# Kernel tuning notes

Hardware: AMD Instinct MI355X
Metric: run time of the kernel (lower is better)

The kernel has to match this reference:

```python
import jax, jax.numpy as jnp
import numpy as np

E = 200_000        # num edges (messages)
T = 2_000_000      # num triplets
H = 128            # hidden_channels
I = 64             # int_emb_size
B = 8              # basis_emb_size
NR = 6             # num_radial
NS = 7             # num_spherical
NB_BEFORE = 1
NB_AFTER = 2


def _glorot(key, shape, scale=2.0):
    fan = shape[0] + shape[1]
    std = jnp.sqrt(scale * 2.0 / fan)
    return jax.random.normal(key, shape, dtype=jnp.float32) * std


def setup_inputs() -> dict:
    key = jax.random.key(0)
    ks = jax.random.split(key, 20)
    inp = {
        "x": jax.random.normal(ks[0], (E, H), dtype=jnp.float32),
        "rbf": jax.random.uniform(ks[1], (E, NR), dtype=jnp.float32),
        "sbf": jax.random.uniform(ks[2], (T, NS * NR), dtype=jnp.float32),
        "idx_kj": jax.random.randint(ks[3], (T,), 0, E),
        "idx_ji": jax.random.randint(ks[4], (T,), 0, E),
        # weights stored as [in, out] so forward is x @ W
        "W_rbf1": _glorot(ks[5], (NR, B)),
        "W_rbf2": _glorot(ks[6], (B, H)),
        "W_sbf1": _glorot(ks[7], (NS * NR, B)),
        "W_sbf2": _glorot(ks[8], (B, I)),
        "W_kj": _glorot(ks[9], (H, H)),
        "b_kj": jnp.zeros((H,), dtype=jnp.float32),
        "W_ji": _glorot(ks[10], (H, H)),
        "b_ji": jnp.zeros((H,), dtype=jnp.float32),
        "W_down": _glorot(ks[11], (H, I)),
        "W_up": _glorot(ks[12], (I, H)),
        # residual layers: [n_layers, 2, H, H] weights, [n_layers, 2, H] biases
        "W_res_before": jnp.stack([jnp.stack([_glorot(jax.random.fold_in(ks[13], 2 * l + m), (H, H)) for m in range(2)]) for l in range(NB_BEFORE)]),
        "b_res_before": jnp.zeros((NB_BEFORE, 2, H), dtype=jnp.float32),
        "W_lin": _glorot(ks[14], (H, H)),
        "b_lin": jnp.zeros((H,), dtype=jnp.float32),
        "W_res_after": jnp.stack([jnp.stack([_glorot(jax.random.fold_in(ks[15], 2 * l + m), (H, H)) for m in range(2)]) for l in range(NB_AFTER)]),
        "b_res_after": jnp.zeros((NB_AFTER, 2, H), dtype=jnp.float32),
    }
    return inp


def _residual_stack(h, Ws, bs):
    # h: [E,H]; Ws: [L,2,H,H]; bs: [L,2,H]
    for l in range(Ws.shape[0]):
        inner = jax.nn.silu(h @ Ws[l, 0] + bs[l, 0])
        h = h + jax.nn.silu(inner @ Ws[l, 1] + bs[l, 1])
    return h


def reference(x, rbf, sbf, idx_kj, idx_ji,
              W_rbf1, W_rbf2, W_sbf1, W_sbf2,
              W_kj, b_kj, W_ji, b_ji, W_down, W_up,
              W_res_before, b_res_before, W_lin, b_lin,
              W_res_after, b_res_after):
    act = jax.nn.silu  # swish
    x_ji = act(x @ W_ji + b_ji)                    # [E,H]
    x_kj = act(x @ W_kj + b_kj)                    # [E,H]
    rbf_e = (rbf @ W_rbf1) @ W_rbf2                # [E,H]
    x_kj = x_kj * rbf_e
    x_kj = act(x_kj @ W_down)                      # [E,I]
    sbf_e = (sbf @ W_sbf1) @ W_sbf2                # [T,I]
    m = x_kj[idx_kj] * sbf_e                       # [T,I] gather + basis weight
    agg = jax.ops.segment_sum(m, idx_ji, num_segments=x.shape[0])  # [E,I] scatter-add
    x_kj = act(agg @ W_up)                         # [E,H]
    h = x_ji + x_kj
    h = _residual_stack(h, W_res_before, b_res_before)
    h = act(h @ W_lin + b_lin) + x                 # skip connection
    h = _residual_stack(h, W_res_after, b_res_after)
    return h
```

## Files before the change

kernel.cpp:

```cpp
#include <hip/hip_runtime.h>
#include <math.h>
#include <stdint.h>

#define SCHUNK 2048
#define PCH 128

typedef __bf16 bf16x8 __attribute__((ext_vector_type(8)));
typedef __bf16 bf16x4 __attribute__((ext_vector_type(4)));
typedef float f32x4 __attribute__((ext_vector_type(4)));

#define MFMA16(a, b, c) __builtin_amdgcn_mfma_f32_16x16x32_bf16(a, b, c, 0, 0, 0)

#define OFF_KJ    0
#define OFF_JI    16384
#define OFF_DOWN  32768
#define OFF_UP    40960
#define OFF_RB0   49152
#define OFF_RB1   65536
#define OFF_LIN   81920
#define OFF_RA00  98304
#define OFF_RA01  114688
#define OFF_RA10  131072
#define OFF_RA11  147456

__device__ __forceinline__ float silu_f(float v) {
    return v * __builtin_amdgcn_rcpf(1.0f + __expf(-v));
}

template<int K, int NB, int NT, int STRIDE, int NTOT>
__device__ __forceinline__ void wgemm(const __bf16* __restrict__ At,
                                      const __bf16* __restrict__ Wf,
                                      int ct0, int lane, f32x4* __restrict__ acc) {
#pragma unroll
    for (int i = 0; i < NB * NT; ++i) acc[i] = (f32x4){0.f, 0.f, 0.f, 0.f};
    const int rl = lane & 15;
    const int kq = (lane >> 4) * 8;
    const int sw = (rl & 7) << 3;
#pragma unroll
    for (int kc = 0; kc < K / 32; ++kc) {
        const int k0 = kc * 32 + kq;
        bf16x8 ef[NB];
#pragma unroll
        for (int s = 0; s < NB; ++s)
            ef[s] = *(const bf16x8*)&At[(rl + 16 * s) * STRIDE + (k0 ^ sw)];
#pragma unroll
        for (int t = 0; t < NT; ++t) {
            bf16x8 wf = *(const bf16x8*)&Wf[(size_t)((kc * NTOT + ct0 + t) * 64 + lane) * 8];
#pragma unroll
            for (int s = 0; s < NB; ++s)
                acc[t * NB + s] = MFMA16(wf, ef[s], acc[t * NB + s]);
        }
    }
}

template<int COLS, int NTHR>
__device__ __forceinline__ void stage(const float* __restrict__ g, long grow0,
                                      int vr, __bf16* __restrict__ At, int tid) {
    constexpr int QUADS = COLS / 4;
#pragma unroll
    for (int i = tid; i < 64 * QUADS; i += NTHR) {
        int r = i / QUADS, q = i - r * QUADS;
        float4 v = make_float4(0.f, 0.f, 0.f, 0.f);
        if (r < vr) v = *(const float4*)&g[(grow0 + r) * (size_t)COLS + q * 4];
        bf16x4 w; w[0] = (__bf16)v.x; w[1] = (__bf16)v.y; w[2] = (__bf16)v.z; w[3] = (__bf16)v.w;
        *(bf16x4*)&At[r * 128 + ((q * 4) ^ ((r & 7) << 3))] = w;
    }
}

template<int COLS, int NTHR>
__device__ __forceinline__ void stage_bf(const __bf16* __restrict__ g, long grow0,
                                         int vr, __bf16* __restrict__ At, int tid) {
    constexpr int CH = COLS / 8;
#pragma unroll
    for (int i = tid; i < 64 * CH; i += NTHR) {
        int r = i / CH, q = i - r * CH;
        bf16x8 v = (bf16x8){0, 0, 0, 0, 0, 0, 0, 0};
        if (r < vr) v = *(const bf16x8*)&g[(grow0 + r) * (size_t)COLS + q * 8];
        *(bf16x8*)&At[r * 128 + ((q * 8) ^ ((r & 7) << 3))] = v;
    }
}

__device__ __forceinline__ void epi_store(__bf16* __restrict__ At, const f32x4* __restrict__ acc,
                                          const float* __restrict__ bias, int lane,
                                          int rowbase, int colbase) {
    const int rl = lane & 15, rg = (lane >> 4) << 2;
#pragma unroll
    for (int t = 0; t < 2; ++t) {
        const int cb = colbase + t * 16 + rg;
        const float4 bv = *(const float4*)&bias[cb];
        const float bb[4] = {bv.x, bv.y, bv.z, bv.w};
#pragma unroll
        for (int s = 0; s < 2; ++s) {
            const int el = rowbase + s * 16 + rl;
            bf16x4 w;
#pragma unroll
            for (int j = 0; j < 4; ++j) w[j] = (__bf16)silu_f(acc[t * 2 + s][j] + bb[j]);
            *(bf16x4*)&At[el * 128 + (cb ^ ((el & 7) << 3))] = w;
        }
    }
}

template<bool WRITE>
__device__ __forceinline__ void epi_add(__bf16* __restrict__ At, f32x4* __restrict__ hreg,
                                        const f32x4* __restrict__ acc,
                                        const float* __restrict__ bias, int lane,
                                        int rowbase, int colbase) {
    const int rl = lane & 15, rg = (lane >> 4) << 2;
#pragma unroll
    for (int t = 0; t < 2; ++t) {
        const int cb = colbase + t * 16 + rg;
        const float4 bv = *(const float4*)&bias[cb];
        const float bb[4] = {bv.x, bv.y, bv.z, bv.w};
#pragma unroll
        for (int s = 0; s < 2; ++s) {
            const int el = rowbase + s * 16 + rl;
            bf16x4 w;
#pragma unroll
            for (int j = 0; j < 4; ++j) {
                float v = hreg[t * 2 + s][j] + silu_f(acc[t * 2 + s][j] + bb[j]);
                hreg[t * 2 + s][j] = v;
                w[j] = (__bf16)v;
            }
            if (WRITE) *(bf16x4*)&At[el * 128 + (cb ^ ((el & 7) << 3))] = w;
        }
    }
}

__global__ void kweights(const float* __restrict__ W_rbf1, const float* __restrict__ W_rbf2,
                         const float* __restrict__ W_sbf1, const float* __restrict__ W_sbf2,
                         float* __restrict__ wcrT, float* __restrict__ wc_sbf,
                         __bf16* __restrict__ wcsb) {
    int tid = blockIdx.x * blockDim.x + threadIdx.x;
    int nt = blockDim.x * gridDim.x;
    for (int idx = tid; idx < 128 * 8; idx += nt) {
        int c = idx >> 3, s = idx & 7;
        float v = 0.f;
        if (s < 6) {
#pragma unroll
            for (int b = 0; b < 8; ++b) v += W_rbf1[s * 8 + b] * W_rbf2[b * 128 + c];
        }
        wcrT[idx] = v;
    }
    for (int idx = tid; idx < 42 * 64; idx += nt) {
        int r = idx / 64, c = idx - r * 64;
        float s = 0.f;
#pragma unroll
        for (int b = 0; b < 8; ++b) s += W_sbf1[r * 8 + b] * W_sbf2[b * 64 + c];
        wc_sbf[idx] = s;
    }
    for (int idx = tid; idx < 4096; idx += nt) {
        int j = idx & 7, l = (idx >> 3) & 63, r2 = idx >> 9;
        int ct = r2 & 3, kc = r2 >> 2;
        int k = kc * 32 + ((l >> 4) << 3) + j;
        int c = ct * 16 + (l & 15);
        float v = 0.f;
        if (k < 42) {
#pragma unroll
            for (int b = 0; b < 8; ++b) v += W_sbf1[k * 8 + b] * W_sbf2[b * 64 + c];
        }
        wcsb[idx] = (__bf16)v;
    }
}

__global__ void ktrans(const float* __restrict__ W_kj, const float* __restrict__ W_ji,
                       const float* __restrict__ W_down, const float* __restrict__ W_up,
                       const float* __restrict__ W_rb, const float* __restrict__ W_lin,
                       const float* __restrict__ W_ra, __bf16* __restrict__ wt) {
    const float* src; __bf16* dst; int K, N;
    switch (blockIdx.y) {
        case 0:  src = W_kj;          dst = wt + OFF_KJ;    K = 128; N = 128; break;
        case 1:  src = W_ji;          dst = wt + OFF_JI;    K = 128; N = 128; break;
        case 2:  src = W_down;        dst = wt + OFF_DOWN;  K = 128; N = 64;  break;
        case 3:  src = W_up;          dst = wt + OFF_UP;    K = 64;  N = 128; break;
        case 4:  src = W_rb;          dst = wt + OFF_RB0;   K = 128; N = 128; break;
        case 5:  src = W_rb + 16384;  dst = wt + OFF_RB1;   K = 128; N = 128; break;
        case 6:  src = W_lin;         dst = wt + OFF_LIN;   K = 128; N = 128; break;
        case 7:  src = W_ra;          dst = wt + OFF_RA00;  K = 128; N = 128; break;
        case 8:  src = W_ra + 16384;  dst = wt + OFF_RA01;  K = 128; N = 128; break;
        case 9:  src = W_ra + 32768;  dst = wt + OFF_RA10;  K = 128; N = 128; break;
        default: src = W_ra + 49152;  dst = wt + OFF_RA11;  K = 128; N = 128; break;
    }
    const int ntot = N / 16;
    for (int i = blockIdx.x * blockDim.x + threadIdx.x; i < K * N; i += gridDim.x * blockDim.x) {
        int j = i & 7, l = (i >> 3) & 63, r2 = i >> 9;
        int ct = r2 % ntot, kc = r2 / ntot;
        int k = kc * 32 + ((l >> 4) << 3) + j;
        int n = ct * 16 + (l & 15);
        dst[i] = (__bf16)src[(size_t)k * N + n];
    }
}

__global__ __launch_bounds__(512, 4) void kpre_m(
        const float* __restrict__ x, const float* __restrict__ rbf,
        const __bf16* __restrict__ wt, const float* __restrict__ b_kj,
        const float* __restrict__ wcrT, __bf16* __restrict__ xkd, int E) {
    __shared__ __bf16 A0[64 * 128];
    __shared__ __bf16 A1[64 * 128];
    __shared__ float rbt[64 * 8];
    const int tid = threadIdx.x, lane = tid & 63, wv = tid >> 6;
    const int rh = wv & 1, cq = wv >> 1;
    const int rowbase = rh * 32, colbase = cq * 32;
    const long r0 = (long)blockIdx.x * 64;
    if (r0 >= E) return;
    const int vr = (E - r0) < 64 ? (int)(E - r0) : 64;
    const int rl = lane & 15, rg = (lane >> 4) << 2;

    stage<128, 512>(x, r0, vr, A0, tid);
    for (int i = tid; i < 64 * 8; i += 512) {
        int r = i >> 3, s = i & 7;
        rbt[i] = (s < 6 && r < vr) ? rbf[(r0 + r) * 6 + s] : 0.f;
    }
    __syncthreads();

    f32x4 acc[4];
    wgemm<128, 2, 2, 128, 8>(A0 + rowbase * 128, wt + OFF_KJ, cq * 2, lane, acc);

#pragma unroll
    for (int t = 0; t < 2; ++t) {
        const int cb = colbase + t * 16 + rg;
        const float4 bv = *(const float4*)&b_kj[cb];
        const float bb[4] = {bv.x, bv.y, bv.z, bv.w};
        float wcr[4][6];
#pragma unroll
        for (int j = 0; j < 4; ++j) {
            float4 a4 = *(const float4*)&wcrT[(cb + j) * 8];
            float2 a2 = *(const float2*)&wcrT[(cb + j) * 8 + 4];
            wcr[j][0] = a4.x; wcr[j][1] = a4.y; wcr[j][2] = a4.z;
            wcr[j][3] = a4.w; wcr[j][4] = a2.x; wcr[j][5] = a2.y;
        }
#pragma unroll
        for (int s = 0; s < 2; ++s) {
            const int el = rowbase + s * 16 + rl;
            float4 r4 = *(const float4*)&rbt[el * 8];
            float2 r2 = *(const float2*)&rbt[el * 8 + 4];
            bf16x4 w;
#pragma unroll
            for (int j = 0; j < 4; ++j) {
                float re = r4.x * wcr[j][0] + r4.y * wcr[j][1] + r4.z * wcr[j][2]
                         + r4.w * wcr[j][3] + r2.x * wcr[j][4] + r2.y * wcr[j][5];
                w[j] = (__bf16)(silu_f(acc[t * 2 + s][j] + bb[j]) * re);
            }
            *(bf16x4*)&A1[el * 128 + (cb ^ ((el & 7) << 3))] = w;
        }
    }
    __syncthreads();

    const int hw = wv >> 2, ct = wv & 3;
    const int cb2 = ct * 16 + rg;
    f32x4 acc2[2];
    wgemm<128, 2, 1, 128, 4>(A1 + hw * 32 * 128, wt + OFF_DOWN, ct, lane, acc2);
#pragma unroll
    for (int s = 0; s < 2; ++s) {
        const int el = hw * 32 + s * 16 + rl;
        if (el < vr) {
            bf16x4 w;
#pragma unroll
            for (int j = 0; j < 4; ++j) w[j] = (__bf16)silu_f(acc2[s][j]);
            *(bf16x4*)&xkd[(r0 + el) * 64 + cb2] = w;
        }
    }
}

__global__ __launch_bounds__(512, 4) void kpost_m(
        const float* __restrict__ x, const __bf16* __restrict__ agg,
        const __bf16* __restrict__ mperm, const int* __restrict__ rs,
        const __bf16* __restrict__ wt, const float* __restrict__ b_ji,
        const float* __restrict__ b_rb, const float* __restrict__ b_lin,
        const float* __restrict__ b_ra, float* __restrict__ out, int E,
        int use_mperm) {
    __shared__ __bf16 A0[64 * 128];
    __shared__ __bf16 A1[64 * 128];
    const int tid = threadIdx.x, lane = tid & 63, wv = tid >> 6;
    const int rh = wv & 1, cq = wv >> 1;
    const int rowbase = rh * 32, colbase = cq * 32;
    const int ct0 = cq * 2;
    const long r0 = (long)blockIdx.x * 64;
    if (r0 >= E) return;
    const int vr = (E - r0) < 64 ? (int)(E - r0) : 64;
    const int rl = lane & 15, rg = (lane >> 4) << 2;
    f32x4 acc[4], hreg[4];

    stage<128, 512>(x, r0, vr, A1, tid);

    if (use_mperm) {
        const int el = tid >> 3, oct = tid & 7;
        const long e = r0 + el;
        float s0[8], s1[8];
#pragma unroll
        for (int k = 0; k < 8; ++k) { s0[k] = 0.f; s1[k] = 0.f; }
        if (el < vr) {
            const int j0 = rs[e], j1 = rs[e + 1];
            const __bf16* pm = mperm + (size_t)j0 * 64 + oct * 8;
            const int n = j1 - j0;
            int j = 0;
            for (; j + 2 <= n; j += 2) {
                bf16x8 v0 = *(const bf16x8*)&pm[(size_t)j * 64];
                bf16x8 v1 = *(const bf16x8*)&pm[(size_t)(j + 1) * 64];
#pragma unroll
                for (int k = 0; k < 8; ++k) { s0[k] += (float)v0[k]; s1[k] += (float)v1[k]; }
            }
            if (j < n) {
                bf16x8 v0 = *(const bf16x8*)&pm[(size_t)j * 64];
#pragma unroll
                for (int k = 0; k < 8; ++k) s0[k] += (float)v0[k];
            }
        }
        bf16x8 w;
#pragma unroll
        for (int k = 0; k < 8; ++k) w[k] = (__bf16)(s0[k] + s1[k]);
        *(bf16x8*)&A0[el * 128 + ((oct * 8) ^ ((el & 7) << 3))] = w;
    } else {
        stage_bf<64, 512>(agg, r0, vr, A0, tid);
    }
    __syncthreads();

    wgemm<64, 2, 2, 128, 8>(A0 + rowbase * 128, wt + OFF_UP, ct0, lane, acc);
#pragma unroll
    for (int i = 0; i < 4; ++i)
#pragma unroll
        for (int j = 0; j < 4; ++j) hreg[i][j] = silu_f(acc[i][j]);
    wgemm<128, 2, 2, 128, 8>(A1 + rowbase * 128, wt + OFF_JI, ct0, lane, acc);
    __syncthreads();
    epi_add<true>(A0, hreg, acc, b_ji, lane, rowbase, colbase);
    __syncthreads();

    wgemm<128, 2, 2, 128, 8>(A0 + rowbase * 128, wt + OFF_RB0, ct0, lane, acc);
    epi_store(A1, acc, b_rb, lane, rowbase, colbase);
    __syncthreads();
    wgemm<128, 2, 2, 128, 8>(A1 + rowbase * 128, wt + OFF_RB1, ct0, lane, acc);
    epi_add<true>(A0, hreg, acc, b_rb + 128, lane, rowbase, colbase);
    __syncthreads();

    wgemm<128, 2, 2, 128, 8>(A0 + rowbase * 128, wt + OFF_LIN, ct0, lane, acc);
#pragma unroll
    for (int t = 0; t < 2; ++t) {
        const int cb = colbase + t * 16 + rg;
        const float4 bv = *(const float4*)&b_lin[cb];
        const float bb[4] = {bv.x, bv.y, bv.z, bv.w};
#pragma unroll
        for (int s = 0; s < 2; ++s) {
            const int el = rowbase + s * 16 + rl;
            float4 xv = make_float4(0.f, 0.f, 0.f, 0.f);
            if (el < vr) xv = *(const float4*)&x[(r0 + el) * 128 + cb];
            const float xx[4] = {xv.x, xv.y, xv.z, xv.w};
            bf16x4 w;
#pragma unroll
            for (int j = 0; j < 4; ++j) {
                float v = silu_f(acc[t * 2 + s][j] + bb[j]) + xx[j];
                hreg[t * 2 + s][j] = v;
                w[j] = (__bf16)v;
            }
            *(bf16x4*)&A1[el * 128 + (cb ^ ((el & 7) << 3))] = w;
        }
    }
    __syncthreads();

    wgemm<128, 2, 2, 128, 8>(A1 + rowbase * 128, wt + OFF_RA00, ct0, lane, acc);
    epi_store(A0, acc, b_ra, lane, rowbase, colbase);
    __syncthreads();
    wgemm<128, 2, 2, 128, 8>(A0 + rowbase * 128, wt + OFF_RA01, ct0, lane, acc);
    epi_add<true>(A1, hreg, acc, b_ra + 128, lane, rowbase, colbase);
    __syncthreads();

    wgemm<128, 2, 2, 128, 8>(A1 + rowbase * 128, wt + OFF_RA10, ct0, lane, acc);
    epi_store(A0, acc, b_ra + 256, lane, rowbase, colbase);
    __syncthreads();
    wgemm<128, 2, 2, 128, 8>(A0 + rowbase * 128, wt + OFF_RA11, ct0, lane, acc);
    epi_add<false>(nullptr, hreg, acc, b_ra + 384, lane, rowbase, colbase);

#pragma unroll
    for (int t = 0; t < 2; ++t) {
        const int cb = colbase + t * 16 + rg;
#pragma unroll
        for (int s = 0; s < 2; ++s) {
            const int el = rowbase + s * 16 + rl;
            if (el < vr) *(f32x4*)&out[(r0 + el) * 128 + cb] = hreg[t * 2 + s];
        }
    }
}

__global__ void khist(const int* __restrict__ idx_ji, int* __restrict__ cnt, int T) {
    int t = blockIdx.x * blockDim.x + threadIdx.x;
    int nt = gridDim.x * blockDim.x;
    for (; t < T; t += nt) atomicAdd(&cnt[idx_ji[t]], 1);
}

__global__ __launch_bounds__(256) void kscan1(int* __restrict__ a, int* __restrict__ bsum) {
    __shared__ int sc[256];
    const int tid = threadIdx.x;
    const int base = blockIdx.x * SCHUNK + tid * 8;
    int4 p0 = *(const int4*)&a[base];
    int4 p1 = *(const int4*)&a[base + 4];
    int v[8] = {p0.x, p0.y, p0.z, p0.w, p1.x, p1.y, p1.z, p1.w};
    int s = 0;
#pragma unroll
    for (int i = 0; i < 8; ++i) s += v[i];
    sc[tid] = s;
    __syncthreads();
    for (int off = 1; off < 256; off <<= 1) {
        int t2 = (tid >= off) ? sc[tid - off] : 0;
        __syncthreads();
        sc[tid] += t2;
        __syncthreads();
    }
    int run = sc[tid] - s;
    if (tid == 255) bsum[blockIdx.x] = sc[255];
    int o[8];
#pragma unroll
    for (int i = 0; i < 8; ++i) { o[i] = run; run += v[i]; }
    *(int4*)&a[base]     = make_int4(o[0], o[1], o[2], o[3]);
    *(int4*)&a[base + 4] = make_int4(o[4], o[5], o[6], o[7]);
}

__global__ void kscan2(int* __restrict__ bsum, int nb) {
    if (threadIdx.x == 0 && blockIdx.x == 0) {
        int run = 0;
        for (int i = 0; i < nb; ++i) { int v = bsum[i]; bsum[i] = run; run += v; }
    }
}

__global__ void kscan3(int* __restrict__ a, const int* __restrict__ bsum,
                       int* __restrict__ cursor, int n) {
    int i = blockIdx.x * blockDim.x + threadIdx.x;
    if (i < n) {
        int v = a[i] + bsum[i >> 11];
        a[i] = v;
        cursor[i] = v;
    }
}

__global__ void kscatter(const int* __restrict__ idx_ji, int* __restrict__ cursor,
                         int* __restrict__ pos, int T) {
    int t = blockIdx.x * blockDim.x + threadIdx.x;
    int nt = gridDim.x * blockDim.x;
    for (; t < T; t += nt) {
        pos[t] = atomicAdd(&cursor[idx_ji[t]], 1);
    }
}

__global__ __launch_bounds__(512, 4) void kperm(
        const float* __restrict__ sbf, const int* __restrict__ idx_kj,
        const int* __restrict__ pos, const __bf16* __restrict__ xkd,
        const __bf16* __restrict__ wcsb, __bf16* __restrict__ mperm, int T) {
    __shared__ __bf16 S[PCH * 64];
    __shared__ __bf16 O[PCH * 72];
    __shared__ int kidx[PCH];
    __shared__ int posv[PCH];
    const int tid = threadIdx.x, lane = tid & 63, wv = tid >> 6;
    const long p0 = (long)blockIdx.x * PCH;
    const int np = (T - p0) > PCH ? PCH : (int)(T - p0);

    for (int i = tid; i < PCH * 64 / 8; i += 512)
        *(bf16x8*)&S[i * 8] = (bf16x8){0, 0, 0, 0, 0, 0, 0, 0};
    for (int i = tid; i < PCH; i += 512) {
        kidx[i] = (i < np) ? idx_kj[p0 + i] : 0;
        posv[i] = (i < np) ? pos[p0 + i] : 0;
    }
    __syncthreads();
    for (int i = tid; i < np * 21; i += 512) {
        int posi = i / 21, q = i - posi * 21;
        float2 v = *(const float2*)&sbf[(p0 + posi) * 42 + 2 * q];
        __bf16* d = &S[posi * 64 + ((2 * q) ^ ((posi & 7) << 3))];
        d[0] = (__bf16)v.x; d[1] = (__bf16)v.y;
    }
    __syncthreads();

    const int rq = wv & 3, cp = wv >> 2;
    f32x4 acc[4];
    wgemm<64, 2, 2, 64, 4>(S + rq * 32 * 64, wcsb, cp * 2, lane, acc);

    const int rl = lane & 15, rg = (lane >> 4) << 2;
#pragma unroll
    for (int t = 0; t < 2; ++t) {
        const int cb = cp * 32 + t * 16 + rg;
#pragma unroll
        for (int s = 0; s < 2; ++s) {
            const int r = rq * 32 + s * 16 + rl;
            const int kj = kidx[r];
            bf16x4 xk = *(const bf16x4*)&xkd[(size_t)kj * 64 + cb];
            bf16x4 w;
#pragma unroll
            for (int j = 0; j < 4; ++j) w[j] = (__bf16)(acc[t * 2 + s][j] * (float)xk[j]);
            *(bf16x4*)&O[r * 72 + cb] = w;
        }
    }
    __syncthreads();

    for (int i = tid; i < np * 8; i += 512) {
        int r = i >> 3, q = i & 7;
        size_t dst = (size_t)posv[r];
        *(bf16x8*)&mperm[dst * 64 + q * 8] = *(const bf16x8*)&O[r * 72 + q * 8];
    }
}

__global__ __launch_bounds__(256) void ktrip(
        const float* __restrict__ sbf, const int* __restrict__ idx_kj,
        const int* __restrict__ idx_ji, const __bf16* __restrict__ xkd,
        const float* __restrict__ wc_sbf, float* __restrict__ aggf, int T) {
    const int lane = threadIdx.x & 63;
    float wc[42];
#pragma unroll
    for (int s = 0; s < 42; ++s) wc[s] = wc_sbf[s * 64 + lane];
    const int wave = blockIdx.x * (blockDim.x >> 6) + (threadIdx.x >> 6);
    const int nw = gridDim.x * (blockDim.x >> 6);
    for (int t = wave; t < T; t += nw) {
        const float* srow = sbf + (size_t)t * 42;
        float acc = 0.f;
#pragma unroll
        for (int q = 0; q < 21; ++q) {
            float2 v = *(const float2*)&srow[q * 2];
            acc = fmaf(v.x, wc[q * 2 + 0], acc);
            acc = fmaf(v.y, wc[q * 2 + 1], acc);
        }
        int kj = idx_kj[t];
        int ji = idx_ji[t];
        float m = (float)xkd[(size_t)kj * 64 + lane] * acc;
        atomicAdd(&aggf[(size_t)ji * 64 + lane], m);
    }
}

__global__ void kcvt(const float* __restrict__ src, __bf16* __restrict__ dst, int n) {
    int i = blockIdx.x * blockDim.x + threadIdx.x;
    int nt = gridDim.x * blockDim.x;
    for (; i < n; i += nt) dst[i] = (__bf16)src[i];
}

static inline char* alignup256(char* p) {
    return (char*)(((uintptr_t)p + 255) & ~(uintptr_t)255);
}

extern "C" void kernel_launch(void* const* d_in, const int* in_sizes, int n_in,
                              void* d_out, int out_size, void* d_ws, size_t ws_size,
                              hipStream_t stream) {
    const float* x      = (const float*)d_in[0];
    const float* rbf    = (const float*)d_in[1];
    const float* sbf    = (const float*)d_in[2];
    const int*   idx_kj = (const int*)d_in[3];
    const int*   idx_ji = (const int*)d_in[4];
    const float* W_rbf1 = (const float*)d_in[5];
    const float* W_rbf2 = (const float*)d_in[6];
    const float* W_sbf1 = (const float*)d_in[7];
    const float* W_sbf2 = (const float*)d_in[8];
    const float* W_kj   = (const float*)d_in[9];
    const float* b_kj   = (const float*)d_in[10];
    const float* W_ji   = (const float*)d_in[11];
    const float* b_ji   = (const float*)d_in[12];
    const float* W_down = (const float*)d_in[13];
    const float* W_up   = (const float*)d_in[14];
    const float* W_rb   = (const float*)d_in[15];
    const float* b_rb   = (const float*)d_in[16];
    const float* W_lin  = (const float*)d_in[17];
    const float* b_lin  = (const float*)d_in[18];
    const float* W_ra   = (const float*)d_in[19];
    const float* b_ra   = (const float*)d_in[20];

    const int E = in_sizes[0] / 128;
    const int T = in_sizes[3];
    const int NB = (E + 1 + SCHUNK - 1) / SCHUNK;
    const int Epad = NB * SCHUNK;

    char* p = (char*)d_ws;
    __bf16* agg  = (__bf16*)p;  p = alignup256(p + (size_t)E * 64 * 2);
    __bf16* xkd  = (__bf16*)p;  p = alignup256(p + (size_t)E * 64 * 2);
    float* wcrT  = (float*)p;   p = alignup256(p + 1024 * 4);
    float* wcs   = (float*)p;   p = alignup256(p + 2688 * 4);
    __bf16* wcsb = (__bf16*)p;  p = alignup256(p + 4096 * 2);
    __bf16* wt   = (__bf16*)p;  p = alignup256(p + (size_t)163840 * 2);
    int* rs      = (int*)p;     p = alignup256(p + (size_t)Epad * 4);
    int* cursor  = (int*)p;     p = alignup256(p + (size_t)Epad * 4);
    int* bsum    = (int*)p;     p = alignup256(p + (size_t)NB * 4);
    int* pos     = (int*)p;     p = alignup256(p + (size_t)T * 4);
    __bf16* mperm = (__bf16*)p; p = alignup256(p + (size_t)T * 64 * 2);
    const bool fits = (size_t)(p - (char*)d_ws) <= ws_size;
    float* aggf = (float*)mperm;
    const bool fits_fb = (size_t)((char*)(aggf + (size_t)E * 64) - (char*)d_ws) <= ws_size;

    kweights<<<16, 256, 0, stream>>>(W_rbf1, W_rbf2, W_sbf1, W_sbf2, wcrT, wcs, wcsb);
    ktrans<<<dim3(16, 11), 256, 0, stream>>>(W_kj, W_ji, W_down, W_up, W_rb, W_lin, W_ra, wt);

    const int gE = (E + 63) / 64;
    kpre_m<<<gE, 512, 0, stream>>>(x, rbf, wt, b_kj, wcrT, xkd, E);

    if (fits) {
        hipMemsetAsync(rs, 0, (size_t)Epad * sizeof(int), stream);
        khist<<<2048, 256, 0, stream>>>(idx_ji, rs, T);
        kscan1<<<NB, 256, 0, stream>>>(rs, bsum);
        kscan2<<<1, 64, 0, stream>>>(bsum, NB);
        kscan3<<<(Epad + 255) / 256, 256, 0, stream>>>(rs, bsum, cursor, Epad);
        kscatter<<<2048, 256, 0, stream>>>(idx_ji, cursor, pos, T);
        kperm<<<(T + PCH - 1) / PCH, 512, 0, stream>>>(sbf, idx_kj, pos, xkd, wcsb, mperm, T);
        kpost_m<<<gE, 512, 0, stream>>>(x, agg, mperm, rs, wt, b_ji, b_rb, b_lin, b_ra,
                                        (float*)d_out, E, 1);
    } else if (fits_fb) {
        hipMemsetAsync(aggf, 0, (size_t)E * 64 * sizeof(float), stream);
        ktrip<<<2048, 256, 0, stream>>>(sbf, idx_kj, idx_ji, xkd, wcs, aggf, T);
        kcvt<<<2048, 256, 0, stream>>>(aggf, agg, E * 64);
        kpost_m<<<gE, 512, 0, stream>>>(x, agg, mperm, rs, wt, b_ji, b_rb, b_lin, b_ra,
                                        (float*)d_out, E, 0);
    }
}
```

Baseline: 622.5 us.

## Shrink edge GEMM tiles to 32 rows, widen swizzle, retile kperm waves

kpre_m and kpost_m now process 32 edge rows per block with 256 threads, each wave owning a 32-column slice of all rows, instead of 64 rows with 512 threads. The aim is more resident blocks per CU and fewer waves idling at each barrier. The LDS XOR swizzle for K=128 tiles is widened from 8 to 16 rows to cut bank conflicts. kperm's GEMM is retiled so each wave covers 64 rows by one 16-column tile, reusing weight fragments across more rows. The cost is that twice as many blocks each re-read the full weight matrices, raising weight traffic through L2.

```diff
diff --git a/kernel.cpp b/kernel.cpp
--- a/kernel.cpp
+++ b/kernel.cpp
@@ -31,11 +31,12 @@
 __device__ __forceinline__ void wgemm(const __bf16* __restrict__ At,
                                       const __bf16* __restrict__ Wf,
                                       int ct0, int lane, f32x4* __restrict__ acc) {
+    constexpr int SWM = (K >= 128) ? 15 : 7;
 #pragma unroll
     for (int i = 0; i < NB * NT; ++i) acc[i] = (f32x4){0.f, 0.f, 0.f, 0.f};
     const int rl = lane & 15;
     const int kq = (lane >> 4) * 8;
-    const int sw = (rl & 7) << 3;
+    const int sw = (rl & SWM) << 3;
 #pragma unroll
     for (int kc = 0; kc < K / 32; ++kc) {
         const int k0 = kc * 32 + kq;
@@ -53,36 +54,31 @@
     }
 }
 
-template<int COLS, int NTHR>
-__device__ __forceinline__ void stage(const float* __restrict__ g, long grow0,
-                                      int vr, __bf16* __restrict__ At, int tid) {
-    constexpr int QUADS = COLS / 4;
-#pragma unroll
-    for (int i = tid; i < 64 * QUADS; i += NTHR) {
-        int r = i / QUADS, q = i - r * QUADS;
+__device__ __forceinline__ void stage32(const float* __restrict__ g, long grow0,
+                                        int vr, __bf16* __restrict__ At, int tid) {
+#pragma unroll
+    for (int i = tid; i < 32 * 32; i += 256) {
+        int r = i >> 5, q = i & 31;
         float4 v = make_float4(0.f, 0.f, 0.f, 0.f);
-        if (r < vr) v = *(const float4*)&g[(grow0 + r) * (size_t)COLS + q * 4];
+        if (r < vr) v = *(const float4*)&g[(grow0 + r) * 128 + q * 4];
         bf16x4 w; w[0] = (__bf16)v.x; w[1] = (__bf16)v.y; w[2] = (__bf16)v.z; w[3] = (__bf16)v.w;
-        *(bf16x4*)&At[r * 128 + ((q * 4) ^ ((r & 7) << 3))] = w;
-    }
-}
-
-template<int COLS, int NTHR>
-__device__ __forceinline__ void stage_bf(const __bf16* __restrict__ g, long grow0,
-                                         int vr, __bf16* __restrict__ At, int tid) {
-    constexpr int CH = COLS / 8;
-#pragma unroll
-    for (int i = tid; i < 64 * CH; i += NTHR) {
-        int r = i / CH, q = i - r * CH;
+        *(bf16x4*)&At[r * 128 + ((q * 4) ^ ((r & 15) << 3))] = w;
+    }
+}
+
+__device__ __forceinline__ void stage_bf32(const __bf16* __restrict__ g, long grow0,
+                                           int vr, __bf16* __restrict__ At, int tid) {
+#pragma unroll
+    for (int i = tid; i < 32 * 8; i += 256) {
+        int r = i >> 3, q = i & 7;
         bf16x8 v = (bf16x8){0, 0, 0, 0, 0, 0, 0, 0};
-        if (r < vr) v = *(const bf16x8*)&g[(grow0 + r) * (size_t)COLS + q * 8];
+        if (r < vr) v = *(const bf16x8*)&g[(grow0 + r) * 64 + q * 8];
         *(bf16x8*)&At[r * 128 + ((q * 8) ^ ((r & 7) << 3))] = v;
     }
 }
 
 __device__ __forceinline__ void epi_store(__bf16* __restrict__ At, const f32x4* __restrict__ acc,
-                                          const float* __restrict__ bias, int lane,
-                                          int rowbase, int colbase) {
+                                          const float* __restrict__ bias, int lane, int colbase) {
     const int rl = lane & 15, rg = (lane >> 4) << 2;
 #pragma unroll
     for (int t = 0; t < 2; ++t) {
@@ -91,11 +87,11 @@
         const float bb[4] = {bv.x, bv.y, bv.z, bv.w};
 #pragma unroll
         for (int s = 0; s < 2; ++s) {
-            const int el = rowbase + s * 16 + rl;
+            const int el = s * 16 + rl;
             bf16x4 w;
 #pragma unroll
             for (int j = 0; j < 4; ++j) w[j] = (__bf16)silu_f(acc[t * 2 + s][j] + bb[j]);
-            *(bf16x4*)&At[el * 128 + (cb ^ ((el & 7) << 3))] = w;
+            *(bf16x4*)&At[el * 128 + (cb ^ ((el & 15) << 3))] = w;
         }
     }
 }
@@ -103,8 +99,7 @@
 template<bool WRITE>
 __device__ __forceinline__ void epi_add(__bf16* __restrict__ At, f32x4* __restrict__ hreg,
                                         const f32x4* __restrict__ acc,
-                                        const float* __restrict__ bias, int lane,
-                                        int rowbase, int colbase) {
+                                        const float* __restrict__ bias, int lane, int colbase) {
     const int rl = lane & 15, rg = (lane >> 4) << 2;
 #pragma unroll
     for (int t = 0; t < 2; ++t) {
@@ -113,7 +108,7 @@
         const float bb[4] = {bv.x, bv.y, bv.z, bv.w};
 #pragma unroll
         for (int s = 0; s < 2; ++s) {
-            const int el = rowbase + s * 16 + rl;
+            const int el = s * 16 + rl;
             bf16x4 w;
 #pragma unroll
             for (int j = 0; j < 4; ++j) {
@@ -121,7 +116,7 @@
                 hreg[t * 2 + s][j] = v;
                 w[j] = (__bf16)v;
             }
-            if (WRITE) *(bf16x4*)&At[el * 128 + (cb ^ ((el & 7) << 3))] = w;
+            if (WRITE) *(bf16x4*)&At[el * 128 + (cb ^ ((el & 15) << 3))] = w;
         }
     }
 }
@@ -190,30 +185,30 @@
     }
 }
 
-__global__ __launch_bounds__(512, 4) void kpre_m(
+__global__ __launch_bounds__(256, 8) void kpre_m(
         const float* __restrict__ x, const float* __restrict__ rbf,
         const __bf16* __restrict__ wt, const float* __restrict__ b_kj,
         const float* __restrict__ wcrT, __bf16* __restrict__ xkd, int E) {
-    __shared__ __bf16 A0[64 * 128];
-    __shared__ __bf16 A1[64 * 128];
-    __shared__ float rbt[64 * 8];
+    __shared__ __bf16 A0[32 * 128];
+    __shared__ __bf16 A1[32 * 128];
+    __shared__ float rbt[32 * 8];
     const int tid = threadIdx.x, lane = tid & 63, wv = tid >> 6;
-    const int rh = wv & 1, cq = wv >> 1;
-    const int rowbase = rh * 32, colbase = cq * 32;
-    const long r0 = (long)blockIdx.x * 64;
+    const int colbase = wv * 32;
+    const long r0 = (long)blockIdx.x * 32;
     if (r0 >= E) return;
-    const int vr = (E - r0) < 64 ? (int)(E - r0) : 64;
+    const int vr = (E - r0) < 32 ? (int)(E - r0) : 32;
     const int rl = lane & 15, rg = (lane >> 4) << 2;
 
-    stage<128, 512>(x, r0, vr, A0, tid);
-    for (int i = tid; i < 64 * 8; i += 512) {
+    stage32(x, r0, vr, A0, tid);
+    if (tid < 256) {
+        int i = tid;
         int r = i >> 3, s = i & 7;
         rbt[i] = (s < 6 && r < vr) ? rbf[(r0 + r) * 6 + s] : 0.f;
     }
     __syncthreads();
 
     f32x4 acc[4];
-    wgemm<128, 2, 2, 128, 8>(A0 + rowbase * 128, wt + OFF_KJ, cq * 2, lane, acc);
+    wgemm<128, 2, 2, 128, 8>(A0, wt + OFF_KJ, wv * 2, lane, acc);
 
 #pragma unroll
     for (int t = 0; t < 2; ++t) {
@@ -230,7 +225,7 @@
         }
 #pragma unroll
         for (int s = 0; s < 2; ++s) {
-            const int el = rowbase + s * 16 + rl;
+            const int el = s * 16 + rl;
             float4 r4 = *(const float4*)&rbt[el * 8];
             float2 r2 = *(const float2*)&rbt[el * 8 + 4];
             bf16x4 w;
@@ -240,18 +235,17 @@
                          + r4.w * wcr[j][3] + r2.x * wcr[j][4] + r2.y * wcr[j][5];
                 w[j] = (__bf16)(silu_f(acc[t * 2 + s][j] + bb[j]) * re);
             }
-            *(bf16x4*)&A1[el * 128 + (cb ^ ((el & 7) << 3))] = w;
-        }
-    }
-    __syncthreads();
-
-    const int hw = wv >> 2, ct = wv & 3;
-    const int cb2 = ct * 16 + rg;
+            *(bf16x4*)&A1[el * 128 + (cb ^ ((el & 15) << 3))] = w;
+        }
+    }
+    __syncthreads();
+
+    const int cb2 = wv * 16 + rg;
     f32x4 acc2[2];
-    wgemm<128, 2, 1, 128, 4>(A1 + hw * 32 * 128, wt + OFF_DOWN, ct, lane, acc2);
+    wgemm<128, 2, 1, 128, 4>(A1, wt + OFF_DOWN, wv, lane, acc2);
 #pragma unroll
     for (int s = 0; s < 2; ++s) {
-        const int el = hw * 32 + s * 16 + rl;
+        const int el = s * 16 + rl;
         if (el < vr) {
             bf16x4 w;
 #pragma unroll
@@ -261,26 +255,25 @@
     }
 }
 
-__global__ __launch_bounds__(512, 4) void kpost_m(
+__global__ __launch_bounds__(256, 8) void kpost_m(
         const float* __restrict__ x, const __bf16* __restrict__ agg,
         const __bf16* __restrict__ mperm, const int* __restrict__ rs,
         const __bf16* __restrict__ wt, const float* __restrict__ b_ji,
         const float* __restrict__ b_rb, const float* __restrict__ b_lin,
         const float* __restrict__ b_ra, float* __restrict__ out, int E,
         int use_mperm) {
-    __shared__ __bf16 A0[64 * 128];
-    __shared__ __bf16 A1[64 * 128];
+    __shared__ __bf16 A0[32 * 128];
+    __shared__ __bf16 A1[32 * 128];
     const int tid = threadIdx.x, lane = tid & 63, wv = tid >> 6;
-    const int rh = wv & 1, cq = wv >> 1;
-    const int rowbase = rh * 32, colbase = cq * 32;
-    const int ct0 = cq * 2;
-    const long r0 = (long)blockIdx.x * 64;
+    const int colbase = wv * 32;
+    const int ct0 = wv * 2;
+    const long r0 = (long)blockIdx.x * 32;
     if (r0 >= E) return;
-    const int vr = (E - r0) < 64 ? (int)(E - r0) : 64;
+    const int vr = (E - r0) < 32 ? (int)(E - r0) : 32;
     const int rl = lane & 15, rg = (lane >> 4) << 2;
     f32x4 acc[4], hreg[4];
 
-    stage<128, 512>(x, r0, vr, A1, tid);
+    stage32(x, r0, vr, A1, tid);
 
     if (use_mperm) {
         const int el = tid >> 3, oct = tid & 7;
@@ -310,28 +303,28 @@
         for (int k = 0; k < 8; ++k) w[k] = (__bf16)(s0[k] + s1[k]);
         *(bf16x8*)&A0[el * 128 + ((oct * 8) ^ ((el & 7) << 3))] = w;
     } else {
-        stage_bf<64, 512>(agg, r0, vr, A0, tid);
-    }
-    __syncthreads();
-
-    wgemm<64, 2, 2, 128, 8>(A0 + rowbase * 128, wt + OFF_UP, ct0, lane, acc);
+        stage_bf32(agg, r0, vr, A0, tid);
+    }
+    __syncthreads();
+
+    wgemm<64, 2, 2, 128, 8>(A0, wt + OFF_UP, ct0, lane, acc);
 #pragma unroll
     for (int i = 0; i < 4; ++i)
 #pragma unroll
         for (int j = 0; j < 4; ++j) hreg[i][j] = silu_f(acc[i][j]);
-    wgemm<128, 2, 2, 128, 8>(A1 + rowbase * 128, wt + OFF_JI, ct0, lane, acc);
-    __syncthreads();
-    epi_add<true>(A0, hreg, acc, b_ji, lane, rowbase, colbase);
-    __syncthreads();
-
-    wgemm<128, 2, 2, 128, 8>(A0 + rowbase * 128, wt + OFF_RB0, ct0, lane, acc);
-    epi_store(A1, acc, b_rb, lane, rowbase, colbase);
-    __syncthreads();
-    wgemm<128, 2, 2, 128, 8>(A1 + rowbase * 128, wt + OFF_RB1, ct0, lane, acc);
-    epi_add<true>(A0, hreg, acc, b_rb + 128, lane, rowbase, colbase);
-    __syncthreads();
-
-    wgemm<128, 2, 2, 128, 8>(A0 + rowbase * 128, wt + OFF_LIN, ct0, lane, acc);
+    wgemm<128, 2, 2, 128, 8>(A1, wt + OFF_JI, ct0, lane, acc);
+    __syncthreads();
+    epi_add<true>(A0, hreg, acc, b_ji, lane, colbase);
+    __syncthreads();
+
+    wgemm<128, 2, 2, 128, 8>(A0, wt + OFF_RB0, ct0, lane, acc);
+    epi_store(A1, acc, b_rb, lane, colbase);
+    __syncthreads();
+    wgemm<128, 2, 2, 128, 8>(A1, wt + OFF_RB1, ct0, lane, acc);
+    epi_add<true>(A0, hreg, acc, b_rb + 128, lane, colbase);
+    __syncthreads();
+
+    wgemm<128, 2, 2, 128, 8>(A0, wt + OFF_LIN, ct0, lane, acc);
 #pragma unroll
     for (int t = 0; t < 2; ++t) {
         const int cb = colbase + t * 16 + rg;
@@ -339,7 +332,7 @@
         const float bb[4] = {bv.x, bv.y, bv.z, bv.w};
 #pragma unroll
         for (int s = 0; s < 2; ++s) {
-            const int el = rowbase + s * 16 + rl;
+            const int el = s * 16 + rl;
             float4 xv = make_float4(0.f, 0.f, 0.f, 0.f);
             if (el < vr) xv = *(const float4*)&x[(r0 + el) * 128 + cb];
             const float xx[4] = {xv.x, xv.y, xv.z, xv.w};
@@ -350,30 +343,30 @@
                 hreg[t * 2 + s][j] = v;
                 w[j] = (__bf16)v;
             }
-            *(bf16x4*)&A1[el * 128 + (cb ^ ((el & 7) << 3))] = w;
-        }
-    }
-    __syncthreads();
-
-    wgemm<128, 2, 2, 128, 8>(A1 + rowbase * 128, wt + OFF_RA00, ct0, lane, acc);
-    epi_store(A0, acc, b_ra, lane, rowbase, colbase);
-    __syncthreads();
-    wgemm<128, 2, 2, 128, 8>(A0 + rowbase * 128, wt + OFF_RA01, ct0, lane, acc);
-    epi_add<true>(A1, hreg, acc, b_ra + 128, lane, rowbase, colbase);
-    __syncthreads();
-
-    wgemm<128, 2, 2, 128, 8>(A1 + rowbase * 128, wt + OFF_RA10, ct0, lane, acc);
-    epi_store(A0, acc, b_ra + 256, lane, rowbase, colbase);
-    __syncthreads();
-    wgemm<128, 2, 2, 128, 8>(A0 + rowbase * 128, wt + OFF_RA11, ct0, lane, acc);
-    epi_add<false>(nullptr, hreg, acc, b_ra + 384, lane, rowbase, colbase);
+            *(bf16x4*)&A1[el * 128 + (cb ^ ((el & 15) << 3))] = w;
+        }
+    }
+    __syncthreads();
+
+    wgemm<128, 2, 2, 128, 8>(A1, wt + OFF_RA00, ct0, lane, acc);
+    epi_store(A0, acc, b_ra, lane, colbase);
+    __syncthreads();
+    wgemm<128, 2, 2, 128, 8>(A0, wt + OFF_RA01, ct0, lane, acc);
+    epi_add<true>(A1, hreg, acc, b_ra + 128, lane, colbase);
+    __syncthreads();
+
+    wgemm<128, 2, 2, 128, 8>(A1, wt + OFF_RA10, ct0, lane, acc);
+    epi_store(A0, acc, b_ra + 256, lane, colbase);
+    __syncthreads();
+    wgemm<128, 2, 2, 128, 8>(A0, wt + OFF_RA11, ct0, lane, acc);
+    epi_add<false>(nullptr, hreg, acc, b_ra + 384, lane, colbase);
 
 #pragma unroll
     for (int t = 0; t < 2; ++t) {
         const int cb = colbase + t * 16 + rg;
 #pragma unroll
         for (int s = 0; s < 2; ++s) {
-            const int el = rowbase + s * 16 + rl;
+            const int el = s * 16 + rl;
             if (el < vr) *(f32x4*)&out[(r0 + el) * 128 + cb] = hreg[t * 2 + s];
         }
     }
@@ -465,24 +458,21 @@
     }
     __syncthreads();
 
-    const int rq = wv & 3, cp = wv >> 2;
+    const int rh = wv & 1, ct = wv >> 1;
     f32x4 acc[4];
-    wgemm<64, 2, 2, 64, 4>(S + rq * 32 * 64, wcsb, cp * 2, lane, acc);
+    wgemm<64, 4, 1, 64, 4>(S + rh * 64 * 64, wcsb, ct, lane, acc);
 
     const int rl = lane & 15, rg = (lane >> 4) << 2;
-#pragma unroll
-    for (int t = 0; t < 2; ++t) {
-        const int cb = cp * 32 + t * 16 + rg;
-#pragma unroll
-        for (int s = 0; s < 2; ++s) {
-            const int r = rq * 32 + s * 16 + rl;
-            const int kj = kidx[r];
-            bf16x4 xk = *(const bf16x4*)&xkd[(size_t)kj * 64 + cb];
-            bf16x4 w;
-#pragma unroll
-            for (int j = 0; j < 4; ++j) w[j] = (__bf16)(acc[t * 2 + s][j] * (float)xk[j]);
-            *(bf16x4*)&O[r * 72 + cb] = w;
-        }
+    const int cb = ct * 16 + rg;
+#pragma unroll
+    for (int s = 0; s < 4; ++s) {
+        const int r = rh * 64 + s * 16 + rl;
+        const int kj = kidx[r];
+        bf16x4 xk = *(const bf16x4*)&xkd[(size_t)kj * 64 + cb];
+        bf16x4 w;
+#pragma unroll
+        for (int j = 0; j < 4; ++j) w[j] = (__bf16)(acc[s][j] * (float)xk[j]);
+        *(bf16x4*)&O[r * 72 + cb] = w;
     }
     __syncthreads();
 
@@ -578,8 +568,8 @@
     kweights<<<16, 256, 0, stream>>>(W_rbf1, W_rbf2, W_sbf1, W_sbf2, wcrT, wcs, wcsb);
     ktrans<<<dim3(16, 11), 256, 0, stream>>>(W_kj, W_ji, W_down, W_up, W_rb, W_lin, W_ra, wt);
 
-    const int gE = (E + 63) / 64;
-    kpre_m<<<gE, 512, 0, stream>>>(x, rbf, wt, b_kj, wcrT, xkd, E);
+    const int gE32 = (E + 31) / 32;
+    kpre_m<<<gE32, 256, 0, stream>>>(x, rbf, wt, b_kj, wcrT, xkd, E);
 
     if (fits) {
         hipMemsetAsync(rs, 0, (size_t)Epad * sizeof(int), stream);
@@ -589,13 +579,13 @@
         kscan3<<<(Epad + 255) / 256, 256, 0, stream>>>(rs, bsum, cursor, Epad);
         kscatter<<<2048, 256, 0, stream>>>(idx_ji, cursor, pos, T);
         kperm<<<(T + PCH - 1) / PCH, 512, 0, stream>>>(sbf, idx_kj, pos, xkd, wcsb, mperm, T);
-        kpost_m<<<gE, 512, 0, stream>>>(x, agg, mperm, rs, wt, b_ji, b_rb, b_lin, b_ra,
-                                        (float*)d_out, E, 1);
+        kpost_m<<<gE32, 256, 0, stream>>>(x, agg, mperm, rs, wt, b_ji, b_rb, b_lin, b_ra,
+                                          (float*)d_out, E, 1);
     } else if (fits_fb) {
         hipMemsetAsync(aggf, 0, (size_t)E * 64 * sizeof(float), stream);
         ktrip<<<2048, 256, 0, stream>>>(sbf, idx_kj, idx_ji, xkd, wcs, aggf, T);
         kcvt<<<2048, 256, 0, stream>>>(aggf, agg, E * 64);
-        kpost_m<<<gE, 512, 0, stream>>>(x, agg, mperm, rs, wt, b_ji, b_rb, b_lin, b_ra,
-                                        (float*)d_out, E, 0);
-    }
-}
+        kpost_m<<<gE32, 256, 0, stream>>>(x, agg, mperm, rs, wt, b_ji, b_rb, b_lin, b_ra,
+                                          (float*)d_out, E, 0);
+    }
+}
```

Measured after the change: 661.4 us. +6.2%, slower.
